# Kernel optimization log

Hardware: AMD Instinct MI355X
Metric: run time of the kernel (lower is better)

Reference implementation:

```python
import jax, jax.numpy as jnp
import numpy as np

G = 16          # spline grid_size
NT = 32         # num_tiles
NS = 2          # num_states
SD = 8          # state_dim
MAXLEN = 2048.0 # max_seq_len
SPREAD = 2.0    # position_spread
LN_EPS = 1e-5


def cubic_bspline(t):
    t = jnp.abs(t)
    r1 = 2.0 / 3.0 - t * t + 0.5 * t ** 3
    r2 = (1.0 / 6.0) * (2.0 - t) ** 3
    return jnp.where(t < 1.0, r1, jnp.where(t < 2.0, r2, jnp.zeros_like(t)))


def ternary(x):
    return jnp.where(x > 0.3, 1.0, jnp.where(x < -0.3, -1.0, 0.0)).astype(x.dtype)


def setup_inputs() -> dict:
    key = jax.random.key(0)
    ks = jax.random.split(key, 14)
    B, T, D = 4, 2048, 1024
    H = D // 4
    x = jax.random.normal(ks[0], (B, T, D), jnp.float32)
    positions = jnp.broadcast_to(jnp.arange(T, dtype=jnp.float32), (B, T))
    states = jax.random.randint(ks[1], (B, T), 0, NS)
    ln_gamma = jnp.ones((D,), jnp.float32)
    ln_beta = jnp.zeros((D,), jnp.float32)
    W1 = jax.random.normal(ks[2], (D, H), jnp.float32) * (1.0 / np.sqrt(D))
    b1 = jnp.zeros((H,), jnp.float32)
    W2 = jax.random.normal(ks[3], (H, 2), jnp.float32) * (1.0 / np.sqrt(H))
    b2 = jnp.zeros((2,), jnp.float32)
    spline_coeffs = jax.random.normal(ks[4], (NT, G, G, 3), jnp.float32) * 0.5
    spline_scales = jnp.ones((NT,), jnp.float32)
    directions = jax.random.normal(ks[5], (NT, D), jnp.float32) * 0.02
    state_signatures = jax.random.normal(ks[6], (NT, SD), jnp.float32) * 0.1
    state_emb = jax.random.normal(ks[7], (NS, SD), jnp.float32)
    state_mod = jnp.ones((NS, NT), jnp.float32)
    output_scale = jnp.ones((1,), jnp.float32) * 0.1
    return dict(x=x, positions=positions, states=states, ln_gamma=ln_gamma,
                ln_beta=ln_beta, W1=W1, b1=b1, W2=W2, b2=b2,
                spline_coeffs=spline_coeffs, spline_scales=spline_scales,
                directions=directions, state_signatures=state_signatures,
                state_emb=state_emb, state_mod=state_mod, output_scale=output_scale)


def reference(x, positions, states, ln_gamma, ln_beta, W1, b1, W2, b2,
              spline_coeffs, spline_scales, directions, state_signatures,
              state_emb, state_mod, output_scale):
    B, T, D = x.shape
    xf = x.reshape(-1, D)                               # [N, D]
    mu = jnp.mean(xf, axis=-1, keepdims=True)
    var = jnp.mean((xf - mu) ** 2, axis=-1, keepdims=True)
    xn = (xf - mu) / jnp.sqrt(var + LN_EPS) * ln_gamma + ln_beta

    # --- three-way routing ---
    sigs = jnp.sign(directions)                         # ternary signatures [NT, D]
    content = xn @ sigs.T                               # [N, NT]
    pos = positions.reshape(-1)
    pn = pos / MAXLEN * NT
    centers = jnp.arange(NT, dtype=xn.dtype)
    spatial = cubic_bspline((pn[:, None] - centers[None, :]) / SPREAD)  # [N, NT]
    st = states.reshape(-1)
    sv = state_emb[st]                                  # [N, SD]
    temporal = jax.nn.sigmoid(sv @ state_signatures.T)  # [N, NT]
    combined = content * spatial * temporal
    probs = jax.nn.softmax(combined * 5.0, axis=-1)
    tile_idx = jnp.argmax(combined, axis=-1)            # [N]
    tile_weights = jnp.take_along_axis(probs, tile_idx[:, None], axis=1)[:, 0]

    # --- compress to 2D spline coordinates ---
    h = jax.nn.gelu(xn @ W1 + b1, approximate=False)
    comp = jnp.tanh(h @ W2 + b2)                        # [N, 2]
    a, b = comp[:, 0], comp[:, 1]

    # --- ternary 2D spline per winning tile (vectorized dispatch) ---
    idx_a = jnp.clip(((a + 1.0) / 2.0 * G).astype(jnp.int32), 0, G - 1)
    idx_b = jnp.clip(((b + 1.0) / 2.0 * G).astype(jnp.int32), 0, G - 1)
    q = spline_coeffs + jax.lax.stop_gradient(ternary(spline_coeffs) - spline_coeffs)
    cell = q[tile_idx, idx_a, idx_b]                    # [N, 3]
    cs = 2.0 / G
    la = (a + 1.0 - idx_a.astype(a.dtype) * cs) / cs
    lb = (b + 1.0 - idx_b.astype(b.dtype) * cs) / cs
    scale = (cell[:, 0] + cell[:, 1] * la + cell[:, 2] * lb) * spline_scales[tile_idx]
    smod = state_mod[st, tile_idx]
    contrib = (scale * smod)[:, None] * directions[tile_idx]  # [N, D]

    out = x + contrib.reshape(B, T, D) * output_scale   # residual, eval (no dropout)
    return out
```

## Files before the change

kernel.cpp:

```cpp
#include <hip/hip_runtime.h>
#include <math.h>

#define NROWS 8192
#define DD    1024
#define HH    256
#define NTT   32
#define NCOLS 288

typedef __attribute__((ext_vector_type(8))) __bf16 bf16x8;
typedef __attribute__((ext_vector_type(4))) float f32x4;
typedef __attribute__((ext_vector_type(8))) unsigned short ushort8_t;

static __device__ __forceinline__ unsigned short f2bf(float f) {
    unsigned int u = __float_as_uint(f);
    unsigned int r = (u + 0x7fffu + ((u >> 16) & 1u)) >> 16;
    return (unsigned short)r;
}

static __device__ __forceinline__ float sgnf(float x) {
    return x > 0.0f ? 1.0f : (x < 0.0f ? -1.0f : 0.0f);
}

static __device__ __forceinline__ float ternf(float x) {
    return x > 0.3f ? 1.0f : (x < -0.3f ? -1.0f : 0.0f);
}

static __device__ __forceinline__ float bspline(float u) {
    float t = fabsf(u);
    if (t < 1.0f) return 0.66666666666666663f - t * t + 0.5f * t * t * t;
    if (t < 2.0f) { float w = 2.0f - t; return 0.16666666666666666f * w * w * w; }
    return 0.0f;
}

__global__ __launch_bounds__(256) void k_prep(const float* __restrict__ W1,
                                              const float* __restrict__ dirs,
                                              const float* __restrict__ gamma,
                                              const float* __restrict__ beta,
                                              unsigned short* __restrict__ WT,
                                              float* __restrict__ colsum,
                                              float* __restrict__ bwv) {
    int bid = blockIdx.x;
    int tid = threadIdx.x;
    if (bid < 256) {
        __shared__ float tile[32][33];
        __shared__ float redg[8][32];
        __shared__ float redb[8][32];
        int ktile = bid & 31;
        int ntile = bid >> 5;
        int tx = tid & 31;
        int ty = tid >> 5;
        float sg = 0.f, sb = 0.f;
#pragma unroll
        for (int i = 0; i < 4; ++i) {
            int k = ktile * 32 + ty + i * 8;
            int n = ntile * 32 + tx;
            float w = W1[(size_t)k * HH + n];
            float gk = gamma[k];
            tile[ty + i * 8][tx] = w * gk;
            sg += w * gk;
            sb += w * beta[k];
        }
        redg[ty][tx] = sg;
        redb[ty][tx] = sb;
        __syncthreads();
#pragma unroll
        for (int i = 0; i < 4; ++i) {
            int n = ntile * 32 + ty + i * 8;
            int k = ktile * 32 + tx;
            WT[(size_t)n * DD + k] = f2bf(tile[tx][ty + i * 8]);
        }
        if (ty == 0) {
            float a = 0.f, c = 0.f;
#pragma unroll
            for (int k = 0; k < 8; ++k) { a += redg[k][tx]; c += redb[k][tx]; }
            int j = ntile * 32 + tx;
            atomicAdd(&colsum[j], a);
            atomicAdd(&bwv[j], c);
        }
    } else {
        int r = bid - 256;
        float4 v  = ((const float4*)(dirs + (size_t)r * DD))[tid];
        float4 g  = ((const float4*)gamma)[tid];
        float4 be = ((const float4*)beta)[tid];
        float s0 = sgnf(v.x), s1 = sgnf(v.y), s2 = sgnf(v.z), s3 = sgnf(v.w);
        ushort4 o;
        o.x = f2bf(s0 * g.x); o.y = f2bf(s1 * g.y);
        o.z = f2bf(s2 * g.z); o.w = f2bf(s3 * g.w);
        ((ushort4*)(WT + (size_t)(HH + r) * DD))[tid] = o;
        float ps = s0 * g.x + s1 * g.y + s2 * g.z + s3 * g.w;
        float pb = s0 * be.x + s1 * be.y + s2 * be.z + s3 * be.w;
#pragma unroll
        for (int off = 32; off; off >>= 1) {
            ps += __shfl_xor(ps, off);
            pb += __shfl_xor(pb, off);
        }
        __shared__ float red[8];
        int wid = tid >> 6, lane = tid & 63;
        if (lane == 0) { red[wid] = ps; red[wid + 4] = pb; }
        __syncthreads();
        if (tid == 0) {
            colsum[HH + r] = red[0] + red[1] + red[2] + red[3];
            bwv[HH + r]    = red[4] + red[5] + red[6] + red[7];
        }
    }
}

__global__ __launch_bounds__(256) void k_gemm(const float* __restrict__ x,
                                              const unsigned short* __restrict__ WT,
                                              const float* __restrict__ colsum,
                                              const float* __restrict__ bwv,
                                              float* __restrict__ HP) {
    __shared__ short Al[2][32 * 64];
    __shared__ short Bl[2][96 * 64];
    __shared__ float stats[32][2];
    int tid = threadIdx.x;
    int colblk = blockIdx.x;
    int rowblk = blockIdx.y;
    int row0  = rowblk * 32;
    int ncol0 = colblk * 96;
    int lane = tid & 63;
    int wid  = tid >> 6;
    int wm = wid >> 1, wn = wid & 1;
    int l15 = lane & 15, l4 = lane >> 4;

    int rA = tid >> 3;
    int c8 = tid & 7;
    const float* xrow = x + (size_t)(row0 + rA) * DD + c8 * 8;
    int abyte = rA * 128 + c8 * 16;
    int aswz  = (rA & 7) << 4;

    float s = 0.f, sq = 0.f;
    f32x4 acc[3];
#pragma unroll
    for (int j = 0; j < 3; ++j) acc[j] = (f32x4){0.f, 0.f, 0.f, 0.f};

#define STAGE(kt, buf)                                                           \
    {                                                                            \
        _Pragma("unroll")                                                        \
        for (int ci = 0; ci < 3; ++ci) {                                         \
            int li = ci * 256 + tid;                                             \
            int r  = li >> 3;                                                    \
            int g  = li & 7;                                                     \
            const unsigned short* src =                                          \
                WT + (size_t)(ncol0 + r) * DD + (kt) * 64 + ((g * 8) ^ ((r & 7) << 3)); \
            __builtin_amdgcn_global_load_lds(                                    \
                (const __attribute__((address_space(1))) void*)(const void*)src, \
                (__attribute__((address_space(3))) void*)(void*)(Bl[buf] + li * 8), \
                16, 0, 0);                                                       \
        }                                                                        \
        float4 v0 = ((const float4*)(xrow + (kt) * 64))[0];                      \
        float4 v1 = ((const float4*)(xrow + (kt) * 64))[1];                      \
        s  += (v0.x + v0.y + v0.z + v0.w) + (v1.x + v1.y + v1.z + v1.w);         \
        sq += (v0.x*v0.x + v0.y*v0.y + v0.z*v0.z + v0.w*v0.w)                    \
            + (v1.x*v1.x + v1.y*v1.y + v1.z*v1.z + v1.w*v1.w);                   \
        ushort8_t w;                                                             \
        w[0] = f2bf(v0.x); w[1] = f2bf(v0.y); w[2] = f2bf(v0.z); w[3] = f2bf(v0.w); \
        w[4] = f2bf(v1.x); w[5] = f2bf(v1.y); w[6] = f2bf(v1.z); w[7] = f2bf(v1.w); \
        *(ushort8_t*)((char*)Al[buf] + (abyte ^ aswz)) = w;                      \
    }

#define COMPUTE(buf)                                                             \
    _Pragma("unroll")                                                            \
    for (int ks = 0; ks < 2; ++ks) {                                             \
        int ra = wm * 16 + l15;                                                  \
        int ca = (ks * 64 + l4 * 16) ^ ((ra & 7) << 4);                          \
        bf16x8 av = *(const bf16x8*)((const char*)Al[buf] + ra * 128 + ca);      \
        bf16x8 bv[3];                                                            \
        _Pragma("unroll")                                                        \
        for (int nf = 0; nf < 3; ++nf) {                                         \
            int rb = wn * 48 + nf * 16 + l15;                                    \
            int cb = (ks * 64 + l4 * 16) ^ ((rb & 7) << 4);                      \
            bv[nf] = *(const bf16x8*)((const char*)Bl[buf] + rb * 128 + cb);     \
        }                                                                        \
        _Pragma("unroll")                                                        \
        for (int nf = 0; nf < 3; ++nf)                                           \
            acc[nf] = __builtin_amdgcn_mfma_f32_16x16x32_bf16(av, bv[nf], acc[nf], 0, 0, 0); \
    }

    STAGE(0, 0);
    __syncthreads();
    for (int kt = 0; kt < 16; ++kt) {
        if (kt < 15) STAGE(kt + 1, (kt + 1) & 1);
        COMPUTE(kt & 1);
        __syncthreads();
    }
#undef STAGE
#undef COMPUTE

    s  += __shfl_xor(s, 1);  s  += __shfl_xor(s, 2);  s  += __shfl_xor(s, 4);
    sq += __shfl_xor(sq, 1); sq += __shfl_xor(sq, 2); sq += __shfl_xor(sq, 4);
    if (c8 == 0) {
        float mu  = s * (1.0f / DD);
        float var = sq * (1.0f / DD) - mu * mu;
        stats[rA][0] = mu;
        stats[rA][1] = rsqrtf(var + 1e-5f);
    }
    __syncthreads();

#pragma unroll
    for (int nf = 0; nf < 3; ++nf) {
        int colg = ncol0 + wn * 48 + nf * 16 + l15;
        float cs = colsum[colg];
        float bw = bwv[colg];
        int rl0 = wm * 16 + l4 * 4;
#pragma unroll
        for (int i = 0; i < 4; ++i) {
            float mu   = stats[rl0 + i][0];
            float rstd = stats[rl0 + i][1];
            HP[(size_t)(row0 + rl0 + i) * NCOLS + colg] =
                rstd * acc[nf][i] - mu * rstd * cs + bw;
        }
    }
}

__global__ __launch_bounds__(256) void k_epilogue(
    const float* __restrict__ HP, const float* __restrict__ x,
    const float* __restrict__ positions, const int* __restrict__ states,
    const float* __restrict__ b1, const float* __restrict__ W2,
    const float* __restrict__ b2, const float* __restrict__ spc,
    const float* __restrict__ sps, const float* __restrict__ dirs,
    const float* __restrict__ ssig, const float* __restrict__ semb,
    const float* __restrict__ smod, const float* __restrict__ oscale,
    float* __restrict__ out) {
    int wid = threadIdx.x >> 6;
    int lane = threadIdx.x & 63;
    int row = blockIdx.x * 4 + wid;

    const float* hrow = HP + (size_t)row * NCOLS;
    float4 hv  = ((const float4*)hrow)[lane];
    float4 b1v = ((const float4*)b1)[lane];
    float hs[4] = {hv.x, hv.y, hv.z, hv.w};
    float bs[4] = {b1v.x, b1v.y, b1v.z, b1v.w};
    float sa = 0.f, sb = 0.f;
#pragma unroll
    for (int i = 0; i < 4; ++i) {
        float h = hs[i] + bs[i];
        float g = 0.5f * h * (1.0f + erff(h * 0.70710678118654752f));
        int j = lane * 4 + i;
        sa += g * W2[2 * j];
        sb += g * W2[2 * j + 1];
    }
#pragma unroll
    for (int off = 32; off; off >>= 1) {
        sa += __shfl_xor(sa, off);
        sb += __shfl_xor(sb, off);
    }
    float av = tanhf(sa + b2[0]);
    float bv = tanhf(sb + b2[1]);

    int st = states[row];
    float comb;
    if (lane < NTT) {
        float content = hrow[HH + lane];
        float pn = positions[row] * ((float)NTT / 2048.0f);
        float u  = (pn - (float)lane) * 0.5f;
        float spv = bspline(u);
        const float* sg = ssig + lane * 8;
        const float* se = semb + st * 8;
        float d0 = 0.f;
#pragma unroll
        for (int k = 0; k < 8; ++k) d0 += se[k] * sg[k];
        float temporal = 1.0f / (1.0f + expf(-d0));
        comb = content * spv * temporal;
    } else {
        comb = -__builtin_inff();
    }
    int bi = lane;
#pragma unroll
    for (int off = 32; off; off >>= 1) {
        float ov = __shfl_xor(comb, off);
        int   oi = __shfl_xor(bi, off);
        if (ov > comb || (ov == comb && oi < bi)) { comb = ov; bi = oi; }
    }
    int ia = (int)((av + 1.0f) * 8.0f); ia = ia < 0 ? 0 : (ia > 15 ? 15 : ia);
    int ib = (int)((bv + 1.0f) * 8.0f); ib = ib < 0 ? 0 : (ib > 15 ? 15 : ib);
    const float* cc = spc + (((size_t)bi * 16 + ia) * 16 + ib) * 3;
    float c0 = ternf(cc[0]), c1 = ternf(cc[1]), c2 = ternf(cc[2]);
    float la = (av + 1.0f - (float)ia * 0.125f) * 8.0f;
    float lb = (bv + 1.0f - (float)ib * 0.125f) * 8.0f;
    float scale = (c0 + c1 * la + c2 * lb) * sps[bi];
    float sm = smod[st * NTT + bi];
    float cr = scale * sm * oscale[0];

    const float4* xr = (const float4*)(x + (size_t)row * DD);
    const float4* dr = (const float4*)(dirs + (size_t)bi * DD);
    float4* orow = (float4*)(out + (size_t)row * DD);
#pragma unroll
    for (int i = 0; i < 4; ++i) {
        int idx = i * 64 + lane;
        float4 xv = xr[idx];
        float4 dv = dr[idx];
        float4 o;
        o.x = fmaf(cr, dv.x, xv.x);
        o.y = fmaf(cr, dv.y, xv.y);
        o.z = fmaf(cr, dv.z, xv.z);
        o.w = fmaf(cr, dv.w, xv.w);
        orow[idx] = o;
    }
}

extern "C" void kernel_launch(void* const* d_in, const int* in_sizes, int n_in,
                              void* d_out, int out_size, void* d_ws, size_t ws_size,
                              hipStream_t stream) {
    const float* x     = (const float*)d_in[0];
    const float* pos   = (const float*)d_in[1];
    const int*   st    = (const int*)d_in[2];
    const float* gam   = (const float*)d_in[3];
    const float* bet   = (const float*)d_in[4];
    const float* W1    = (const float*)d_in[5];
    const float* b1    = (const float*)d_in[6];
    const float* W2    = (const float*)d_in[7];
    const float* b2    = (const float*)d_in[8];
    const float* spc   = (const float*)d_in[9];
    const float* sps   = (const float*)d_in[10];
    const float* dirs  = (const float*)d_in[11];
    const float* ssig  = (const float*)d_in[12];
    const float* semb  = (const float*)d_in[13];
    const float* smod  = (const float*)d_in[14];
    const float* oscal = (const float*)d_in[15];
    float* out = (float*)d_out;

    char* ws = (char*)d_ws;
    unsigned short* WT = (unsigned short*)ws;
    float* colsum = (float*)(ws + 589824);
    float* bwv    = (float*)(ws + 589824 + 288 * 4);
    float* HP     = (float*)(ws + 1048576);

    hipMemsetAsync(colsum, 0, 2 * 288 * sizeof(float), stream);
    k_prep<<<288, 256, 0, stream>>>(W1, dirs, gam, bet, WT, colsum, bwv);
    k_gemm<<<dim3(3, 256), 256, 0, stream>>>(x, WT, colsum, bwv, HP);
    k_epilogue<<<NROWS / 4, 256, 0, stream>>>(HP, x, pos, st, b1, W2, b2, spc, sps,
                                              dirs, ssig, semb, smod, oscal, out);
}
```

Before: 46.01 us.

## Prefetch x two stages ahead and pipeline GEMM main loop with explicit waitcnts

```diff
diff --git a/kernel.cpp b/kernel.cpp
--- a/kernel.cpp
+++ b/kernel.cpp
@@ -126,15 +126,15 @@
     int rA = tid >> 3;
     int c8 = tid & 7;
     const float* xrow = x + (size_t)(row0 + rA) * DD + c8 * 8;
-    int abyte = rA * 128 + c8 * 16;
-    int aswz  = (rA & 7) << 4;
+    int abyte = (rA * 128 + c8 * 16) ^ ((rA & 7) << 4);
 
     float s = 0.f, sq = 0.f;
+    float4 x0a, x0b, x1a, x1b;
     f32x4 acc[3];
 #pragma unroll
     for (int j = 0; j < 3; ++j) acc[j] = (f32x4){0.f, 0.f, 0.f, 0.f};
 
-#define STAGE(kt, buf)                                                           \
+#define STAGE_B(kt, buf)                                                         \
     {                                                                            \
         _Pragma("unroll")                                                        \
         for (int ci = 0; ci < 3; ++ci) {                                         \
@@ -148,44 +148,77 @@
                 (__attribute__((address_space(3))) void*)(void*)(Bl[buf] + li * 8), \
                 16, 0, 0);                                                       \
         }                                                                        \
-        float4 v0 = ((const float4*)(xrow + (kt) * 64))[0];                      \
-        float4 v1 = ((const float4*)(xrow + (kt) * 64))[1];                      \
-        s  += (v0.x + v0.y + v0.z + v0.w) + (v1.x + v1.y + v1.z + v1.w);         \
-        sq += (v0.x*v0.x + v0.y*v0.y + v0.z*v0.z + v0.w*v0.w)                    \
-            + (v1.x*v1.x + v1.y*v1.y + v1.z*v1.z + v1.w*v1.w);                   \
-        ushort8_t w;                                                             \
-        w[0] = f2bf(v0.x); w[1] = f2bf(v0.y); w[2] = f2bf(v0.z); w[3] = f2bf(v0.w); \
-        w[4] = f2bf(v1.x); w[5] = f2bf(v1.y); w[6] = f2bf(v1.z); w[7] = f2bf(v1.w); \
-        *(ushort8_t*)((char*)Al[buf] + (abyte ^ aswz)) = w;                      \
-    }
-
-#define COMPUTE(buf)                                                             \
+    }
+
+#define WRITE_A(XA, XB, buf)                                                    \
+    {                                                                           \
+        s  += (XA.x + XA.y + XA.z + XA.w) + (XB.x + XB.y + XB.z + XB.w);        \
+        sq += (XA.x*XA.x + XA.y*XA.y + XA.z*XA.z + XA.w*XA.w)                   \
+            + (XB.x*XB.x + XB.y*XB.y + XB.z*XB.z + XB.w*XB.w);                  \
+        ushort8_t w;                                                            \
+        w[0] = f2bf(XA.x); w[1] = f2bf(XA.y); w[2] = f2bf(XA.z); w[3] = f2bf(XA.w); \
+        w[4] = f2bf(XB.x); w[5] = f2bf(XB.y); w[6] = f2bf(XB.z); w[7] = f2bf(XB.w); \
+        *(ushort8_t*)((char*)Al[buf] + abyte) = w;                              \
+    }
+
+#define COMPUTE(CUR)                                                             \
     _Pragma("unroll")                                                            \
     for (int ks = 0; ks < 2; ++ks) {                                             \
         int ra = wm * 16 + l15;                                                  \
         int ca = (ks * 64 + l4 * 16) ^ ((ra & 7) << 4);                          \
-        bf16x8 av = *(const bf16x8*)((const char*)Al[buf] + ra * 128 + ca);      \
+        bf16x8 av = *(const bf16x8*)((const char*)Al[CUR] + ra * 128 + ca);      \
         bf16x8 bv[3];                                                            \
         _Pragma("unroll")                                                        \
         for (int nf = 0; nf < 3; ++nf) {                                         \
             int rb = wn * 48 + nf * 16 + l15;                                    \
             int cb = (ks * 64 + l4 * 16) ^ ((rb & 7) << 4);                      \
-            bv[nf] = *(const bf16x8*)((const char*)Bl[buf] + rb * 128 + cb);     \
+            bv[nf] = *(const bf16x8*)((const char*)Bl[CUR] + rb * 128 + cb);     \
         }                                                                        \
         _Pragma("unroll")                                                        \
         for (int nf = 0; nf < 3; ++nf)                                           \
             acc[nf] = __builtin_amdgcn_mfma_f32_16x16x32_bf16(av, bv[nf], acc[nf], 0, 0, 0); \
     }
 
-    STAGE(0, 0);
-    __syncthreads();
-    for (int kt = 0; kt < 16; ++kt) {
-        if (kt < 15) STAGE(kt + 1, (kt + 1) & 1);
-        COMPUTE(kt & 1);
-        __syncthreads();
-    }
-#undef STAGE
+#define STEP(kt, XCa, XCb, XIa, XIb, CUR, NXT)                                  \
+    {                                                                           \
+        if ((kt) <= 14) STAGE_B((kt) + 1, NXT);                                 \
+        __builtin_amdgcn_sched_barrier(0);                                      \
+        if ((kt) <= 13) {                                                       \
+            XIa = ((const float4*)(xrow + ((kt) + 2) * 64))[0];                 \
+            XIb = ((const float4*)(xrow + ((kt) + 2) * 64))[1];                 \
+        }                                                                       \
+        COMPUTE(CUR);                                                           \
+        if ((kt) <= 14) WRITE_A(XCa, XCb, NXT);                                 \
+        if ((kt) <= 13) {                                                       \
+            asm volatile("s_waitcnt vmcnt(2) lgkmcnt(0)" ::: "memory");         \
+        } else if ((kt) == 14) {                                                \
+            asm volatile("s_waitcnt vmcnt(0) lgkmcnt(0)" ::: "memory");         \
+        }                                                                       \
+        if ((kt) <= 14) {                                                       \
+            __builtin_amdgcn_s_barrier();                                       \
+            __builtin_amdgcn_sched_barrier(0);                                  \
+        }                                                                       \
+    }
+
+    STAGE_B(0, 0);
+    __builtin_amdgcn_sched_barrier(0);
+    x0a = ((const float4*)(xrow))[0];
+    x0b = ((const float4*)(xrow))[1];
+    x1a = ((const float4*)(xrow + 64))[0];
+    x1b = ((const float4*)(xrow + 64))[1];
+    WRITE_A(x0a, x0b, 0);
+    asm volatile("s_waitcnt vmcnt(2) lgkmcnt(0)" ::: "memory");
+    __builtin_amdgcn_s_barrier();
+    __builtin_amdgcn_sched_barrier(0);
+
+    for (int kt = 0; kt < 16; kt += 2) {
+        STEP(kt,     x1a, x1b, x0a, x0b, 0, 1);
+        STEP(kt + 1, x0a, x0b, x1a, x1b, 1, 0);
+    }
+#undef STAGE_B
+#undef WRITE_A
 #undef COMPUTE
+#undef STEP
 
     s  += __shfl_xor(s, 1);  s  += __shfl_xor(s, 2);  s  += __shfl_xor(s, 4);
     sq += __shfl_xor(sq, 1); sq += __shfl_xor(sq, 2); sq += __shfl_xor(sq, 4);
```

Result: no change. 46.16 us (+0.3%).

## Retile fused LN-GEMM to 16-row blocks with six waves and swizzled block order

Applied to the files above, without the earlier changes.

```diff
diff --git a/kernel.cpp b/kernel.cpp
--- a/kernel.cpp
+++ b/kernel.cpp
@@ -105,40 +105,39 @@
     }
 }
 
-__global__ __launch_bounds__(256) void k_gemm(const float* __restrict__ x,
-                                              const unsigned short* __restrict__ WT,
-                                              const float* __restrict__ colsum,
-                                              const float* __restrict__ bwv,
-                                              float* __restrict__ HP) {
-    __shared__ short Al[2][32 * 64];
+#define GTHR 384
+__global__ __launch_bounds__(GTHR, 6) void k_gemm(const float* __restrict__ x,
+                                                  const unsigned short* __restrict__ WT,
+                                                  const float* __restrict__ colsum,
+                                                  const float* __restrict__ bwv,
+                                                  float* __restrict__ HP) {
+    __shared__ short Al[2][16 * 64];
     __shared__ short Bl[2][96 * 64];
-    __shared__ float stats[32][2];
+    __shared__ float stats[16][2];
     int tid = threadIdx.x;
-    int colblk = blockIdx.x;
-    int rowblk = blockIdx.y;
-    int row0  = rowblk * 32;
+    int bid = blockIdx.y * 3 + blockIdx.x;
+    int swz = (bid & 7) * 192 + (bid >> 3);
+    int colblk = swz % 3;
+    int rowblk = swz / 3;
+    int row0  = rowblk * 16;
     int ncol0 = colblk * 96;
     int lane = tid & 63;
     int wid  = tid >> 6;
-    int wm = wid >> 1, wn = wid & 1;
     int l15 = lane & 15, l4 = lane >> 4;
 
-    int rA = tid >> 3;
+    int rA = (tid >> 3) & 15;
     int c8 = tid & 7;
     const float* xrow = x + (size_t)(row0 + rA) * DD + c8 * 8;
-    int abyte = rA * 128 + c8 * 16;
-    int aswz  = (rA & 7) << 4;
+    int abyte = (rA * 128 + c8 * 16) ^ ((rA & 7) << 4);
 
     float s = 0.f, sq = 0.f;
-    f32x4 acc[3];
-#pragma unroll
-    for (int j = 0; j < 3; ++j) acc[j] = (f32x4){0.f, 0.f, 0.f, 0.f};
+    f32x4 acc = (f32x4){0.f, 0.f, 0.f, 0.f};
 
 #define STAGE(kt, buf)                                                           \
     {                                                                            \
         _Pragma("unroll")                                                        \
-        for (int ci = 0; ci < 3; ++ci) {                                         \
-            int li = ci * 256 + tid;                                             \
+        for (int ci = 0; ci < 2; ++ci) {                                         \
+            int li = ci * GTHR + tid;                                            \
             int r  = li >> 3;                                                    \
             int g  = li & 7;                                                     \
             const unsigned short* src =                                          \
@@ -148,33 +147,28 @@
                 (__attribute__((address_space(3))) void*)(void*)(Bl[buf] + li * 8), \
                 16, 0, 0);                                                       \
         }                                                                        \
-        float4 v0 = ((const float4*)(xrow + (kt) * 64))[0];                      \
-        float4 v1 = ((const float4*)(xrow + (kt) * 64))[1];                      \
-        s  += (v0.x + v0.y + v0.z + v0.w) + (v1.x + v1.y + v1.z + v1.w);         \
-        sq += (v0.x*v0.x + v0.y*v0.y + v0.z*v0.z + v0.w*v0.w)                    \
-            + (v1.x*v1.x + v1.y*v1.y + v1.z*v1.z + v1.w*v1.w);                   \
-        ushort8_t w;                                                             \
-        w[0] = f2bf(v0.x); w[1] = f2bf(v0.y); w[2] = f2bf(v0.z); w[3] = f2bf(v0.w); \
-        w[4] = f2bf(v1.x); w[5] = f2bf(v1.y); w[6] = f2bf(v1.z); w[7] = f2bf(v1.w); \
-        *(ushort8_t*)((char*)Al[buf] + (abyte ^ aswz)) = w;                      \
+        if (tid < 128) {                                                         \
+            float4 v0 = ((const float4*)(xrow + (kt) * 64))[0];                  \
+            float4 v1 = ((const float4*)(xrow + (kt) * 64))[1];                  \
+            s  += (v0.x + v0.y + v0.z + v0.w) + (v1.x + v1.y + v1.z + v1.w);     \
+            sq += (v0.x*v0.x + v0.y*v0.y + v0.z*v0.z + v0.w*v0.w)                \
+                + (v1.x*v1.x + v1.y*v1.y + v1.z*v1.z + v1.w*v1.w);               \
+            ushort8_t w;                                                         \
+            w[0] = f2bf(v0.x); w[1] = f2bf(v0.y); w[2] = f2bf(v0.z); w[3] = f2bf(v0.w); \
+            w[4] = f2bf(v1.x); w[5] = f2bf(v1.y); w[6] = f2bf(v1.z); w[7] = f2bf(v1.w); \
+            *(ushort8_t*)((char*)Al[buf] + abyte) = w;                           \
+        }                                                                        \
     }
 
 #define COMPUTE(buf)                                                             \
     _Pragma("unroll")                                                            \
     for (int ks = 0; ks < 2; ++ks) {                                             \
-        int ra = wm * 16 + l15;                                                  \
-        int ca = (ks * 64 + l4 * 16) ^ ((ra & 7) << 4);                          \
-        bf16x8 av = *(const bf16x8*)((const char*)Al[buf] + ra * 128 + ca);      \
-        bf16x8 bv[3];                                                            \
-        _Pragma("unroll")                                                        \
-        for (int nf = 0; nf < 3; ++nf) {                                         \
-            int rb = wn * 48 + nf * 16 + l15;                                    \
-            int cb = (ks * 64 + l4 * 16) ^ ((rb & 7) << 4);                      \
-            bv[nf] = *(const bf16x8*)((const char*)Bl[buf] + rb * 128 + cb);     \
-        }                                                                        \
-        _Pragma("unroll")                                                        \
-        for (int nf = 0; nf < 3; ++nf)                                           \
-            acc[nf] = __builtin_amdgcn_mfma_f32_16x16x32_bf16(av, bv[nf], acc[nf], 0, 0, 0); \
+        int ca = (ks * 64 + l4 * 16) ^ ((l15 & 7) << 4);                         \
+        bf16x8 av = *(const bf16x8*)((const char*)Al[buf] + l15 * 128 + ca);     \
+        int rb = wid * 16 + l15;                                                 \
+        int cb = (ks * 64 + l4 * 16) ^ ((rb & 7) << 4);                          \
+        bf16x8 bv = *(const bf16x8*)((const char*)Bl[buf] + rb * 128 + cb);      \
+        acc = __builtin_amdgcn_mfma_f32_16x16x32_bf16(av, bv, acc, 0, 0, 0);     \
     }
 
     STAGE(0, 0);
@@ -187,28 +181,29 @@
 #undef STAGE
 #undef COMPUTE
 
-    s  += __shfl_xor(s, 1);  s  += __shfl_xor(s, 2);  s  += __shfl_xor(s, 4);
-    sq += __shfl_xor(sq, 1); sq += __shfl_xor(sq, 2); sq += __shfl_xor(sq, 4);
-    if (c8 == 0) {
-        float mu  = s * (1.0f / DD);
-        float var = sq * (1.0f / DD) - mu * mu;
-        stats[rA][0] = mu;
-        stats[rA][1] = rsqrtf(var + 1e-5f);
+    if (tid < 128) {
+        s  += __shfl_xor(s, 1);  s  += __shfl_xor(s, 2);  s  += __shfl_xor(s, 4);
+        sq += __shfl_xor(sq, 1); sq += __shfl_xor(sq, 2); sq += __shfl_xor(sq, 4);
+        if (c8 == 0) {
+            float mu  = s * (1.0f / DD);
+            float var = sq * (1.0f / DD) - mu * mu;
+            stats[rA][0] = mu;
+            stats[rA][1] = rsqrtf(var + 1e-5f);
+        }
     }
     __syncthreads();
 
-#pragma unroll
-    for (int nf = 0; nf < 3; ++nf) {
-        int colg = ncol0 + wn * 48 + nf * 16 + l15;
+    {
+        int colg = ncol0 + wid * 16 + l15;
         float cs = colsum[colg];
         float bw = bwv[colg];
-        int rl0 = wm * 16 + l4 * 4;
+        int rl0 = l4 * 4;
 #pragma unroll
         for (int i = 0; i < 4; ++i) {
             float mu   = stats[rl0 + i][0];
             float rstd = stats[rl0 + i][1];
             HP[(size_t)(row0 + rl0 + i) * NCOLS + colg] =
-                rstd * acc[nf][i] - mu * rstd * cs + bw;
+                rstd * acc[i] - mu * rstd * cs + bw;
         }
     }
 }
@@ -328,7 +323,7 @@
 
     hipMemsetAsync(colsum, 0, 2 * 288 * sizeof(float), stream);
     k_prep<<<288, 256, 0, stream>>>(W1, dirs, gam, bet, WT, colsum, bwv);
-    k_gemm<<<dim3(3, 256), 256, 0, stream>>>(x, WT, colsum, bwv, HP);
+    k_gemm<<<dim3(3, 512), GTHR, 0, stream>>>(x, WT, colsum, bwv, HP);
     k_epilogue<<<NROWS / 4, 256, 0, stream>>>(HP, x, pos, st, b1, W2, b2, spc, sps,
                                               dirs, ssig, semb, smod, oscal, out);
 }
```

New measurement: 51.46 us. +11.8%, slower.

## Move LayerNorm into prep kernel writing bf16 normalized activations for GEMM

Applied to the files above, without the earlier changes.

```diff
diff --git a/kernel.cpp b/kernel.cpp
--- a/kernel.cpp
+++ b/kernel.cpp
@@ -9,7 +9,6 @@
 
 typedef __attribute__((ext_vector_type(8))) __bf16 bf16x8;
 typedef __attribute__((ext_vector_type(4))) float f32x4;
-typedef __attribute__((ext_vector_type(8))) unsigned short ushort8_t;
 
 static __device__ __forceinline__ unsigned short f2bf(float f) {
     unsigned int u = __float_as_uint(f);
@@ -32,36 +31,27 @@
     return 0.0f;
 }
 
-__global__ __launch_bounds__(256) void k_prep(const float* __restrict__ W1,
-                                              const float* __restrict__ dirs,
-                                              const float* __restrict__ gamma,
-                                              const float* __restrict__ beta,
-                                              unsigned short* __restrict__ WT,
-                                              float* __restrict__ colsum,
-                                              float* __restrict__ bwv) {
+__global__ __launch_bounds__(256) void k_prep_ln(const float* __restrict__ W1,
+                                                 const float* __restrict__ dirs,
+                                                 const float* __restrict__ gamma,
+                                                 const float* __restrict__ beta,
+                                                 const float* __restrict__ x,
+                                                 unsigned short* __restrict__ WT,
+                                                 unsigned short* __restrict__ XN) {
     int bid = blockIdx.x;
     int tid = threadIdx.x;
     if (bid < 256) {
         __shared__ float tile[32][33];
-        __shared__ float redg[8][32];
-        __shared__ float redb[8][32];
         int ktile = bid & 31;
         int ntile = bid >> 5;
         int tx = tid & 31;
         int ty = tid >> 5;
-        float sg = 0.f, sb = 0.f;
 #pragma unroll
         for (int i = 0; i < 4; ++i) {
             int k = ktile * 32 + ty + i * 8;
             int n = ntile * 32 + tx;
-            float w = W1[(size_t)k * HH + n];
-            float gk = gamma[k];
-            tile[ty + i * 8][tx] = w * gk;
-            sg += w * gk;
-            sb += w * beta[k];
+            tile[ty + i * 8][tx] = W1[(size_t)k * HH + n];
         }
-        redg[ty][tx] = sg;
-        redb[ty][tx] = sb;
         __syncthreads();
 #pragma unroll
         for (int i = 0; i < 4; ++i) {
@@ -69,53 +59,54 @@
             int k = ktile * 32 + tx;
             WT[(size_t)n * DD + k] = f2bf(tile[tx][ty + i * 8]);
         }
-        if (ty == 0) {
-            float a = 0.f, c = 0.f;
-#pragma unroll
-            for (int k = 0; k < 8; ++k) { a += redg[k][tx]; c += redb[k][tx]; }
-            int j = ntile * 32 + tx;
-            atomicAdd(&colsum[j], a);
-            atomicAdd(&bwv[j], c);
-        }
+    } else if (bid < 288) {
+        int r = bid - 256;
+        float4 v = ((const float4*)(dirs + (size_t)r * DD))[tid];
+        ushort4 o;
+        o.x = f2bf(sgnf(v.x)); o.y = f2bf(sgnf(v.y));
+        o.z = f2bf(sgnf(v.z)); o.w = f2bf(sgnf(v.w));
+        ((ushort4*)(WT + (size_t)(HH + r) * DD))[tid] = o;
     } else {
-        int r = bid - 256;
-        float4 v  = ((const float4*)(dirs + (size_t)r * DD))[tid];
-        float4 g  = ((const float4*)gamma)[tid];
-        float4 be = ((const float4*)beta)[tid];
-        float s0 = sgnf(v.x), s1 = sgnf(v.y), s2 = sgnf(v.z), s3 = sgnf(v.w);
-        ushort4 o;
-        o.x = f2bf(s0 * g.x); o.y = f2bf(s1 * g.y);
-        o.z = f2bf(s2 * g.z); o.w = f2bf(s3 * g.w);
-        ((ushort4*)(WT + (size_t)(HH + r) * DD))[tid] = o;
-        float ps = s0 * g.x + s1 * g.y + s2 * g.z + s3 * g.w;
-        float pb = s0 * be.x + s1 * be.y + s2 * be.z + s3 * be.w;
+        int row = bid - 288;
+        const float4* xr = (const float4*)(x + (size_t)row * DD);
+        float4 v = xr[tid];
+        float s  = v.x + v.y + v.z + v.w;
+        float sq = v.x * v.x + v.y * v.y + v.z * v.z + v.w * v.w;
 #pragma unroll
         for (int off = 32; off; off >>= 1) {
-            ps += __shfl_xor(ps, off);
-            pb += __shfl_xor(pb, off);
+            s  += __shfl_xor(s, off);
+            sq += __shfl_xor(sq, off);
         }
         __shared__ float red[8];
         int wid = tid >> 6, lane = tid & 63;
-        if (lane == 0) { red[wid] = ps; red[wid + 4] = pb; }
+        if (lane == 0) { red[wid] = s; red[wid + 4] = sq; }
         __syncthreads();
-        if (tid == 0) {
-            colsum[HH + r] = red[0] + red[1] + red[2] + red[3];
-            bwv[HH + r]    = red[4] + red[5] + red[6] + red[7];
-        }
-    }
-}
-
-__global__ __launch_bounds__(256) void k_gemm(const float* __restrict__ x,
+        s  = red[0] + red[1] + red[2] + red[3];
+        sq = red[4] + red[5] + red[6] + red[7];
+        float mu   = s * (1.0f / DD);
+        float var  = sq * (1.0f / DD) - mu * mu;
+        float rstd = rsqrtf(var + 1e-5f);
+        float4 gm = ((const float4*)gamma)[tid];
+        float4 bt = ((const float4*)beta)[tid];
+        ushort4 o;
+        o.x = f2bf((v.x - mu) * rstd * gm.x + bt.x);
+        o.y = f2bf((v.y - mu) * rstd * gm.y + bt.y);
+        o.z = f2bf((v.z - mu) * rstd * gm.z + bt.z);
+        o.w = f2bf((v.w - mu) * rstd * gm.w + bt.w);
+        ((ushort4*)(XN + (size_t)row * DD))[tid] = o;
+    }
+}
+
+__global__ __launch_bounds__(256) void k_gemm(const unsigned short* __restrict__ XN,
                                               const unsigned short* __restrict__ WT,
-                                              const float* __restrict__ colsum,
-                                              const float* __restrict__ bwv,
                                               float* __restrict__ HP) {
     __shared__ short Al[2][32 * 64];
     __shared__ short Bl[2][96 * 64];
-    __shared__ float stats[32][2];
     int tid = threadIdx.x;
-    int colblk = blockIdx.x;
-    int rowblk = blockIdx.y;
+    int bid = blockIdx.x;
+    int swz = (bid & 7) * 96 + (bid >> 3);
+    int colblk = swz % 3;
+    int rowblk = swz / 3;
     int row0  = rowblk * 32;
     int ncol0 = colblk * 96;
     int lane = tid & 63;
@@ -123,19 +114,23 @@
     int wm = wid >> 1, wn = wid & 1;
     int l15 = lane & 15, l4 = lane >> 4;
 
-    int rA = tid >> 3;
-    int c8 = tid & 7;
-    const float* xrow = x + (size_t)(row0 + rA) * DD + c8 * 8;
-    int abyte = rA * 128 + c8 * 16;
-    int aswz  = (rA & 7) << 4;
-
-    float s = 0.f, sq = 0.f;
     f32x4 acc[3];
 #pragma unroll
     for (int j = 0; j < 3; ++j) acc[j] = (f32x4){0.f, 0.f, 0.f, 0.f};
 
 #define STAGE(kt, buf)                                                           \
     {                                                                            \
+                           \
+        {                                                                        \
+            int r = tid >> 3, g = tid & 7;                                       \
+            const unsigned short* srcA =                                         \
+                XN + (size_t)(row0 + r) * DD + (kt) * 64 + ((g * 8) ^ ((r & 7) << 3)); \
+            __builtin_amdgcn_global_load_lds(                                    \
+                (const __attribute__((address_space(1))) void*)(const void*)srcA,\
+                (__attribute__((address_space(3))) void*)(void*)(Al[buf] + tid * 8), \
+                16, 0, 0);                                                       \
+        }                                                                        \
+                                            \
         _Pragma("unroll")                                                        \
         for (int ci = 0; ci < 3; ++ci) {                                         \
             int li = ci * 256 + tid;                                             \
@@ -148,15 +143,6 @@
                 (__attribute__((address_space(3))) void*)(void*)(Bl[buf] + li * 8), \
                 16, 0, 0);                                                       \
         }                                                                        \
-        float4 v0 = ((const float4*)(xrow + (kt) * 64))[0];                      \
-        float4 v1 = ((const float4*)(xrow + (kt) * 64))[1];                      \
-        s  += (v0.x + v0.y + v0.z + v0.w) + (v1.x + v1.y + v1.z + v1.w);         \
-        sq += (v0.x*v0.x + v0.y*v0.y + v0.z*v0.z + v0.w*v0.w)                    \
-            + (v1.x*v1.x + v1.y*v1.y + v1.z*v1.z + v1.w*v1.w);                   \
-        ushort8_t w;                                                             \
-        w[0] = f2bf(v0.x); w[1] = f2bf(v0.y); w[2] = f2bf(v0.z); w[3] = f2bf(v0.w); \
-        w[4] = f2bf(v1.x); w[5] = f2bf(v1.y); w[6] = f2bf(v1.z); w[7] = f2bf(v1.w); \
-        *(ushort8_t*)((char*)Al[buf] + (abyte ^ aswz)) = w;                      \
     }
 
 #define COMPUTE(buf)                                                             \
@@ -187,28 +173,13 @@
 #undef STAGE
 #undef COMPUTE
 
-    s  += __shfl_xor(s, 1);  s  += __shfl_xor(s, 2);  s  += __shfl_xor(s, 4);
-    sq += __shfl_xor(sq, 1); sq += __shfl_xor(sq, 2); sq += __shfl_xor(sq, 4);
-    if (c8 == 0) {
-        float mu  = s * (1.0f / DD);
-        float var = sq * (1.0f / DD) - mu * mu;
-        stats[rA][0] = mu;
-        stats[rA][1] = rsqrtf(var + 1e-5f);
-    }
-    __syncthreads();
-
 #pragma unroll
     for (int nf = 0; nf < 3; ++nf) {
         int colg = ncol0 + wn * 48 + nf * 16 + l15;
-        float cs = colsum[colg];
-        float bw = bwv[colg];
         int rl0 = wm * 16 + l4 * 4;
 #pragma unroll
         for (int i = 0; i < 4; ++i) {
-            float mu   = stats[rl0 + i][0];
-            float rstd = stats[rl0 + i][1];
-            HP[(size_t)(row0 + rl0 + i) * NCOLS + colg] =
-                rstd * acc[nf][i] - mu * rstd * cs + bw;
+            HP[(size_t)(row0 + rl0 + i) * NCOLS + colg] = acc[nf][i];
         }
     }
 }
@@ -322,13 +293,11 @@
 
     char* ws = (char*)d_ws;
     unsigned short* WT = (unsigned short*)ws;
-    float* colsum = (float*)(ws + 589824);
-    float* bwv    = (float*)(ws + 589824 + 288 * 4);
-    float* HP     = (float*)(ws + 1048576);
-
-    hipMemsetAsync(colsum, 0, 2 * 288 * sizeof(float), stream);
-    k_prep<<<288, 256, 0, stream>>>(W1, dirs, gam, bet, WT, colsum, bwv);
-    k_gemm<<<dim3(3, 256), 256, 0, stream>>>(x, WT, colsum, bwv, HP);
+    unsigned short* XN = (unsigned short*)(ws + 1048576);
+    float* HP          = (float*)(ws + 1048576 + 16777216);
+
+    k_prep_ln<<<288 + NROWS, 256, 0, stream>>>(W1, dirs, gam, bet, x, WT, XN);
+    k_gemm<<<768, 256, 0, stream>>>(XN, WT, HP);
     k_epilogue<<<NROWS / 4, 256, 0, stream>>>(HP, x, pos, st, b1, W2, b2, spc, sps,
                                               dirs, ssig, semb, smod, oscal, out);
 }
```

Result: slower. 48.02 us (+4.4%).
